# Kernel tuning notes

Hardware: AMD Instinct MI355X
Metric: run time of the kernel (lower is better)

Reference implementation:

```python
import jax, jax.numpy as jnp
import numpy as np

VOCAB = 32000
D = 512
H = 8
B = 1
SEQ = 4096
CHUNK = 1024  # max_len == chunk size


def _pe(seq, d):
    pos = np.arange(seq, dtype=np.float32)[:, None]
    div = np.exp(np.arange(0, d, 2, dtype=np.float32) * (-np.log(10000.0) / d))
    pe = np.zeros((seq, d), dtype=np.float32)
    pe[:, 0::2] = np.sin(pos * div)
    pe[:, 1::2] = np.cos(pos * div)
    return jnp.asarray(pe)


def _mha(x, w_in, b_in, w_out, b_out, h):
    # x: (..., L, d); attention along L, batched over leading dims.
    lead = x.shape[:-2]
    L, d = x.shape[-2], x.shape[-1]
    hd = d // h
    qkv = x @ w_in.T + b_in                      # (..., L, 3d)
    q, k, v = jnp.split(qkv, 3, axis=-1)
    q = q.reshape(lead + (L, h, hd))
    k = k.reshape(lead + (L, h, hd))
    v = v.reshape(lead + (L, h, hd))
    scores = jnp.einsum('...qhd,...khd->...hqk', q, k) * (1.0 / np.sqrt(hd))
    attn = jax.nn.softmax(scores, axis=-1)
    o = jnp.einsum('...hqk,...khd->...qhd', attn, v).reshape(lead + (L, d))
    return o @ w_out.T + b_out


def _ln(x, g, b, eps=1e-5):
    m = x.mean(-1, keepdims=True)
    v = x.var(-1, keepdims=True)
    return (x - m) / jnp.sqrt(v + eps) * g + b


def setup_inputs() -> dict:
    key = jax.random.key(0)
    ks = jax.random.split(key, 10)
    n = lambda k, s: jax.random.normal(k, s, jnp.float32) * 0.02
    return {
        'tokens': jax.random.randint(ks[0], (B, SEQ), 0, VOCAB),
        'emb': n(ks[1], (VOCAB, D)),
        'chunk_w_in': n(ks[2], (3 * D, D)), 'chunk_b_in': jnp.zeros((3 * D,), jnp.float32),
        'chunk_w_out': n(ks[3], (D, D)), 'chunk_b_out': jnp.zeros((D,), jnp.float32),
        'glob_w_in': n(ks[4], (3 * D, D)), 'glob_b_in': jnp.zeros((3 * D,), jnp.float32),
        'glob_w_out': n(ks[5], (D, D)), 'glob_b_out': jnp.zeros((D,), jnp.float32),
        'ln1_g': jnp.ones((D,), jnp.float32), 'ln1_b': jnp.zeros((D,), jnp.float32),
        'ffn_w1': n(ks[6], (4 * D, D)), 'ffn_b1': jnp.zeros((4 * D,), jnp.float32),
        'ffn_w2': n(ks[7], (D, 4 * D)), 'ffn_b2': jnp.zeros((D,), jnp.float32),
        'ln2_g': jnp.ones((D,), jnp.float32), 'ln2_b': jnp.zeros((D,), jnp.float32),
        'fc_w': n(ks[8], (VOCAB, D)), 'fc_b': jnp.zeros((VOCAB,), jnp.float32),
    }


def reference(tokens, emb, chunk_w_in, chunk_b_in, chunk_w_out, chunk_b_out,
              glob_w_in, glob_b_in, glob_w_out, glob_b_out,
              ln1_g, ln1_b, ffn_w1, ffn_b1, ffn_w2, ffn_b2,
              ln2_g, ln2_b, fc_w, fc_b):
    # embedding * sqrt(d) + sinusoidal positional encoding (dropout in eval = identity)
    x = emb[tokens] * np.sqrt(D).astype(np.float32) + _pe(SEQ, D)[None]  # (B, S, d)
    b, s, d = x.shape
    nc = s // CHUNK
    # BeamSplitter chunk stage: attend across the nc chunks at each intra-chunk position
    xc = x.reshape(b, nc, CHUNK, d).transpose(0, 2, 1, 3)   # (B, CHUNK, nc, d)
    ca = _mha(xc, chunk_w_in, chunk_b_in, chunk_w_out, chunk_b_out, H)
    ca = ca.transpose(0, 2, 1, 3).reshape(b, s, d)          # (B, S, d)
    # global stage: full attention over the sequence
    ga = _mha(ca, glob_w_in, glob_b_in, glob_w_out, glob_b_out, H)
    # post-norm transformer encoder layer
    x = _ln(x + ga, ln1_g, ln1_b)
    f = jax.nn.relu(x @ ffn_w1.T + ffn_b1) @ ffn_w2.T + ffn_b2
    x = _ln(x + f, ln2_g, ln2_b)
    return x @ fc_w.T + fc_b                                 # (B, S, VOCAB)
```

## Files before the change

kernel.cpp:

```cpp
#include <hip/hip_runtime.h>

typedef __attribute__((ext_vector_type(8))) short bf16x8;
typedef __attribute__((ext_vector_type(4))) float f32x4;
typedef unsigned short u16;

__device__ __forceinline__ u16 f2b(float f) {
  union { float f; unsigned u; } v; v.f = f;
  return (u16)((v.u + 0x7FFFu + ((v.u >> 16) & 1u)) >> 16);
}
__device__ __forceinline__ float b2f(u16 x) {
  union { unsigned u; float f; } v; v.u = (unsigned)x << 16; return v.f;
}

__device__ __forceinline__ void gload16(const void* g, void* l) {
  __builtin_amdgcn_global_load_lds((__attribute__((address_space(1))) void*)(g),
                                   (__attribute__((address_space(3))) void*)(l),
                                   16, 0, 0);
}

__device__ __forceinline__ void mbar() {
  asm volatile("" ::: "memory");
  __builtin_amdgcn_s_barrier();
  asm volatile("" ::: "memory");
}

__device__ __forceinline__ void cv1(const float4* __restrict__ s, u16* __restrict__ d, int i) {
  float4 v = s[i];
  unsigned long long pk = (unsigned long long)f2b(v.x) |
                          ((unsigned long long)f2b(v.y) << 16) |
                          ((unsigned long long)f2b(v.z) << 32) |
                          ((unsigned long long)f2b(v.w) << 48);
  *(unsigned long long*)(d + (size_t)i * 4) = pk;
}

__global__ __launch_bounds__(256)
void f2b_multi(const float4* s0, u16* d0, const float4* s1, u16* d1,
               const float4* s2, u16* d2, const float4* s3, u16* d3,
               const float4* s4, u16* d4, const float4* s5, u16* d5,
               const float4* s6, u16* d6) {
  int i = blockIdx.x * 256 + threadIdx.x;
  const int stride = gridDim.x * 256;
  for (; i < 5144576; i += stride) {
    int j = i;
    if (j < 196608) { cv1(s0, d0, j); continue; }
    j -= 196608;
    if (j < 65536) { cv1(s1, d1, j); continue; }
    j -= 65536;
    if (j < 196608) { cv1(s2, d2, j); continue; }
    j -= 196608;
    if (j < 65536) { cv1(s3, d3, j); continue; }
    j -= 65536;
    if (j < 262144) { cv1(s4, d4, j); continue; }
    j -= 262144;
    if (j < 262144) { cv1(s5, d5, j); continue; }
    j -= 262144;
    cv1(s6, d6, j);
  }
}

__global__ __launch_bounds__(256) void embed_pe(const int* __restrict__ tok,
    const float* __restrict__ emb, float* __restrict__ xf, u16* __restrict__ xb) {
  const int s = blockIdx.x;
  const int i = threadIdx.x;
  const int t = tok[s];
  const float div = __expf((float)(2 * i) * -0.017988946039015984f);
  const float ang = (float)s * div;
  const float sv = sinf(ang), cv = cosf(ang);
  const float* e = emb + (size_t)t * 512 + 2 * i;
  const float x0 = e[0] * 22.627416997969522f + sv;
  const float x1 = e[1] * 22.627416997969522f + cv;
  const size_t o = (size_t)s * 512 + 2 * i;
  xf[o] = x0; xf[o + 1] = x1;
  xb[o] = f2b(x0); xb[o + 1] = f2b(x1);
}

template<int BM, int RELU, int WF32, int WB16>
__global__ __launch_bounds__(256)
void gemm_bt(const u16* __restrict__ A, const u16* __restrict__ B,
             const float* __restrict__ bias, float* __restrict__ Cf,
             u16* __restrict__ Cb, int M, int N, int K)
{
  constexpr int MFR = BM / 32;
  __shared__ __align__(16) u16 As[BM * 64];
  __shared__ __align__(16) u16 Bs[128 * 64];
  const int tid = threadIdx.x;
  const int wid = tid >> 6, lane = tid & 63;
  const int lo = lane & 15, hi = lane >> 4;
  const int nbn = N >> 7;
  const int cpx = (int)gridDim.x >> 3;
  const int bid = blockIdx.x;
  const int swz = (bid & 7) * cpx + (bid >> 3);
  const int bi = swz / nbn, bj = swz - bi * nbn;
  const size_t row0 = (size_t)bi * BM, col0 = (size_t)bj << 7;
  const int wr = (wid >> 1) * (BM / 2), wc = (wid & 1) << 6;
  const int srow = (wid << 3) + (lane >> 3);
  const int scol = ((lane & 7) ^ (lane >> 3)) << 3;

  f32x4 acc[MFR][4] = {};

  auto rdA = [&](int row, int ks) -> bf16x8 {
    return *(const bf16x8*)((const char*)As + row * 128 + ((((ks << 2) | hi) ^ (row & 7)) << 4));
  };
  auto rdB = [&](int row, int ks) -> bf16x8 {
    return *(const bf16x8*)((const char*)Bs + row * 128 + ((((ks << 2) | hi) ^ (row & 7)) << 4));
  };

  for (int k0 = 0; k0 < K; k0 += 64) {
    __syncthreads();
#pragma unroll
    for (int p = 0; p < BM / 32; ++p)
      gload16(A + (row0 + srow + 32 * p) * (size_t)K + k0 + scol, &As[(wid * 8 + 32 * p) * 64]);
#pragma unroll
    for (int p = 0; p < 4; ++p)
      gload16(B + (col0 + srow + 32 * p) * (size_t)K + k0 + scol, &Bs[(wid * 8 + 32 * p) * 64]);
    __syncthreads();
#pragma unroll
    for (int ks = 0; ks < 2; ++ks) {
      bf16x8 af[MFR], bfr[4];
#pragma unroll
      for (int m = 0; m < MFR; ++m) af[m] = rdA(wr + m * 16 + lo, ks);
#pragma unroll
      for (int n = 0; n < 4; ++n) bfr[n] = rdB(wc + n * 16 + lo, ks);
#pragma unroll
      for (int m = 0; m < MFR; ++m)
#pragma unroll
        for (int n = 0; n < 4; ++n)
          acc[m][n] = __builtin_amdgcn_mfma_f32_16x16x32_bf16(af[m], bfr[n], acc[m][n], 0, 0, 0);
    }
  }

#pragma unroll
  for (int m = 0; m < MFR; ++m)
#pragma unroll
    for (int n = 0; n < 4; ++n) {
      const size_t c = col0 + wc + n * 16 + lo;
      const float bv = bias[c];
#pragma unroll
      for (int i = 0; i < 4; ++i) {
        const size_t r = row0 + wr + m * 16 + hi * 4 + i;
        float v = acc[m][n][i] + bv;
        if (RELU) v = fmaxf(v, 0.0f);
        if (WF32) Cf[r * (size_t)N + c] = v;
        if (WB16) Cb[r * (size_t)N + c] = f2b(v);
      }
    }
}

template<int KC>
__global__ __launch_bounds__(512, 2)
void gemm256(const u16* __restrict__ A, const u16* __restrict__ B,
             const float* __restrict__ bias, float* __restrict__ C,
             int M, int N)
{
  constexpr int T = KC / 64;
  __shared__ __align__(16) u16 LA[2][256 * 64];
  __shared__ __align__(16) u16 LB[2][256 * 64];
  const int tid = threadIdx.x;
  const int wid = tid >> 6, lane = tid & 63;
  const int lo = lane & 15, hi = lane >> 4;
  const int nbn = N >> 8;
  const int cpx = (int)gridDim.x >> 3;
  const int bid = blockIdx.x;
  const int swz = (bid & 7) * cpx + (bid >> 3);
  const int bi = swz / nbn, bj = swz - bi * nbn;
  const size_t row0 = (size_t)bi << 8, col0 = (size_t)bj << 8;
  const int wrow = (wid >> 2) << 7;
  const int wcol = (wid & 3) << 6;

  const int srow = (wid << 3) + (lane >> 3);
  const int scol = ((lane & 7) ^ (lane >> 3)) << 3;
  const u16* srcA = A + (row0 + srow) * (size_t)KC + scol;
  const u16* srcB = B + (col0 + srow) * (size_t)KC + scol;
  const int ldst = wid << 9;

  f32x4 acc[8][4] = {};

  auto stage = [&](int t, int b) {
    const size_t ko = (size_t)t * 64;
#pragma unroll
    for (int i = 0; i < 4; ++i)
      gload16(srcA + ko + (size_t)(i * 64) * KC, &LA[b][ldst + i * 4096]);
#pragma unroll
    for (int i = 0; i < 4; ++i)
      gload16(srcB + ko + (size_t)(i * 64) * KC, &LB[b][ldst + i * 4096]);
  };

  auto rd = [&](const u16* base, int row, int ks) -> bf16x8 {
    const int byte = row * 128 + ((((ks << 2) | hi) ^ (row & 7)) << 4);
    return *(const bf16x8*)((const char*)base + byte);
  };

  stage(0, 0);
  stage(1, 1);

  for (int t = 0; t < T; ++t) {
    const int b = t & 1;
    const u16* Ab = LA[b];
    const u16* Bb = LB[b];
    if (t + 1 < T) { asm volatile("s_waitcnt vmcnt(8)" ::: "memory"); }
    else           { asm volatile("s_waitcnt vmcnt(0)" ::: "memory"); }
    __builtin_amdgcn_sched_barrier(0);
    mbar();

    bf16x8 afr[4], bfr[4];
#pragma unroll
    for (int ks = 0; ks < 2; ++ks) {
#pragma unroll
      for (int m = 0; m < 4; ++m) afr[m] = rd(Ab, wrow + m * 16 + lo, ks);
#pragma unroll
      for (int n = 0; n < 4; ++n) bfr[n] = rd(Bb, wcol + n * 16 + lo, ks);
      mbar();
      asm volatile("s_waitcnt lgkmcnt(0)" ::: "memory");
      __builtin_amdgcn_sched_barrier(0);
      __builtin_amdgcn_s_setprio(1);
#pragma unroll
      for (int m = 0; m < 4; ++m)
#pragma unroll
        for (int n = 0; n < 4; ++n)
          acc[m][n] = __builtin_amdgcn_mfma_f32_16x16x32_bf16(afr[m], bfr[n], acc[m][n], 0, 0, 0);
      __builtin_amdgcn_s_setprio(0);
      mbar();
#pragma unroll
      for (int m = 0; m < 4; ++m) afr[m] = rd(Ab, wrow + (4 + m) * 16 + lo, ks);
      mbar();
      asm volatile("s_waitcnt lgkmcnt(0)" ::: "memory");
      __builtin_amdgcn_sched_barrier(0);
      __builtin_amdgcn_s_setprio(1);
#pragma unroll
      for (int m = 0; m < 4; ++m)
#pragma unroll
        for (int n = 0; n < 4; ++n)
          acc[4 + m][n] = __builtin_amdgcn_mfma_f32_16x16x32_bf16(afr[m], bfr[n], acc[4 + m][n], 0, 0, 0);
      __builtin_amdgcn_s_setprio(0);
      mbar();
    }
    if (t + 2 < T) stage(t + 2, b);
  }

#pragma unroll
  for (int m = 0; m < 8; ++m)
#pragma unroll
    for (int n = 0; n < 4; ++n) {
      const size_t c = col0 + wcol + n * 16 + lo;
      const float bv = bias[c];
#pragma unroll
      for (int i = 0; i < 4; ++i) {
        const size_t r = row0 + wrow + m * 16 + hi * 4 + i;
        C[r * (size_t)N + c] = acc[m][n][i] + bv;
      }
    }
}

__global__ __launch_bounds__(64)
void chunk_attn(const u16* __restrict__ qkv, u16* __restrict__ out) {
  const int p = blockIdx.x, h = blockIdx.y, d = threadIdx.x;
  float q[4], k[4], v[4];
#pragma unroll
  for (int c = 0; c < 4; ++c) {
    const u16* b = qkv + (size_t)((c << 10) + p) * 1536 + (h << 6) + d;
    q[c] = b2f(b[0]); k[c] = b2f(b[512]); v[c] = b2f(b[1024]);
  }
  float sc[4][4];
#pragma unroll
  for (int i = 0; i < 4; ++i)
#pragma unroll
    for (int j = 0; j < 4; ++j) sc[i][j] = q[i] * k[j];
#pragma unroll
  for (int mask = 1; mask < 64; mask <<= 1)
#pragma unroll
    for (int i = 0; i < 4; ++i)
#pragma unroll
      for (int j = 0; j < 4; ++j) sc[i][j] += __shfl_xor(sc[i][j], mask);
#pragma unroll
  for (int i = 0; i < 4; ++i) {
    float s0 = sc[i][0] * 0.125f, s1 = sc[i][1] * 0.125f,
          s2 = sc[i][2] * 0.125f, s3 = sc[i][3] * 0.125f;
    const float mx = fmaxf(fmaxf(s0, s1), fmaxf(s2, s3));
    const float e0 = __expf(s0 - mx), e1 = __expf(s1 - mx),
                e2 = __expf(s2 - mx), e3 = __expf(s3 - mx);
    const float inv = 1.0f / (e0 + e1 + e2 + e3);
    const float o = (e0 * v[0] + e1 * v[1] + e2 * v[2] + e3 * v[3]) * inv;
    out[(size_t)((i << 10) + p) * 512 + (h << 6) + d] = f2b(o);
  }
}

__global__ __launch_bounds__(512)
void flash_attn(const u16* __restrict__ qkv, u16* __restrict__ out) {
  __shared__ __align__(16) u16 Ks[64 * 64];
  __shared__ __align__(16) u16 Vt[64 * 64];
  __shared__ __align__(16) u16 Pp[8][16 * 64];
  const int tid = threadIdx.x, wid = tid >> 6, lane = tid & 63;
  const int lo = lane & 15, hi = lane >> 4;
  const int q0 = blockIdx.x << 7, h = blockIdx.y;
  const int hoff = h << 6;
  char* KsB = (char*)Ks; char* VtB = (char*)Vt;
  char* Pw = (char*)&Pp[wid][0];
  const int xsw = (lo & 7) << 4;
  constexpr float C1 = 0.18033688011112042f;

  bf16x8 qf[2];
#pragma unroll
  for (int kh = 0; kh < 2; ++kh)
    qf[kh] = *(const bf16x8*)(qkv + (size_t)(q0 + wid * 16 + lo) * 1536 + hoff + kh * 32 + hi * 8);

  f32x4 o[4] = {};
  float mr = -3e38f, lr = 0.f;

  const int krow = tid >> 3, kq = tid & 7;

  bf16x8 kpre = *(const bf16x8*)(qkv + (size_t)krow * 1536 + 512 + hoff + kq * 8);
  bf16x8 vpre = *(const bf16x8*)(qkv + (size_t)krow * 1536 + 1024 + hoff + kq * 8);

  for (int kv0 = 0; kv0 < 4096; kv0 += 64) {
    __syncthreads();
    *(bf16x8*)(KsB + ((krow * 128 + kq * 16) ^ ((krow & 7) << 4))) = kpre;
    {
      const unsigned* vp = (const unsigned*)&vpre;
      const int oddr = krow & 1;
      const unsigned t0 = oddr ? vp[0] : vp[2];
      const unsigned t1 = oddr ? vp[1] : vp[3];
      const unsigned r0 = (unsigned)__shfl_xor((int)t0, 8);
      const unsigned r1 = (unsigned)__shfl_xor((int)t1, 8);
      const unsigned E0 = oddr ? r0 : vp[0];
      const unsigned E1 = oddr ? r1 : vp[1];
      const unsigned O0 = oddr ? vp[2] : r0;
      const unsigned O1 = oddr ? vp[3] : r1;
      const int jp = krow & ~1;
      const int db = kq * 8 + oddr * 4;
      unsigned w0 = (E0 & 0xffffu) | (O0 << 16);
      unsigned w1 = (E0 >> 16) | (O0 & 0xffff0000u);
      unsigned w2 = (E1 & 0xffffu) | (O1 << 16);
      unsigned w3 = (E1 >> 16) | (O1 & 0xffff0000u);
      *(unsigned*)(VtB + (((db + 0) * 128 + 2 * jp) ^ (((db + 0) & 7) << 4))) = w0;
      *(unsigned*)(VtB + (((db + 1) * 128 + 2 * jp) ^ (((db + 1) & 7) << 4))) = w1;
      *(unsigned*)(VtB + (((db + 2) * 128 + 2 * jp) ^ (((db + 2) & 7) << 4))) = w2;
      *(unsigned*)(VtB + (((db + 3) * 128 + 2 * jp) ^ (((db + 3) & 7) << 4))) = w3;
    }
    __syncthreads();
    if (kv0 + 64 < 4096) {
      kpre = *(const bf16x8*)(qkv + (size_t)(kv0 + 64 + krow) * 1536 + 512 + hoff + kq * 8);
      vpre = *(const bf16x8*)(qkv + (size_t)(kv0 + 64 + krow) * 1536 + 1024 + hoff + kq * 8);
    }

    f32x4 s[4] = {};
#pragma unroll
    for (int n = 0; n < 4; ++n) {
      const int key = n * 16 + lo;
#pragma unroll
      for (int kh = 0; kh < 2; ++kh) {
        bf16x8 kf = *(const bf16x8*)(KsB + ((key * 128 + kh * 64 + hi * 16) ^ ((key & 7) << 4)));
        s[n] = __builtin_amdgcn_mfma_f32_16x16x32_bf16(kf, qf[kh], s[n], 0, 0, 0);
      }
    }

    float pm = s[0][0];
#pragma unroll
    for (int n = 0; n < 4; ++n)
#pragma unroll
      for (int i = 0; i < 4; ++i) pm = fmaxf(pm, s[n][i]);
    pm = fmaxf(pm, __shfl_xor(pm, 16));
    pm = fmaxf(pm, __shfl_xor(pm, 32));

    if (__any(pm > mr + 64.f)) {
      const float mn = fmaxf(mr, pm);
      const float sc = exp2f((mr - mn) * C1);
      mr = mn;
      lr *= sc;
#pragma unroll
      for (int i = 0; i < 4; ++i) {
        const float sq = __shfl(sc, hi * 4 + i);
#pragma unroll
        for (int n = 0; n < 4; ++n) o[n][i] *= sq;
      }
    }

    const float mc = mr * C1;
    float rs = 0.f;
    unsigned U[8];
#pragma unroll
    for (int n = 0; n < 4; ++n) {
      const float p0 = exp2f(fmaf(s[n][0], C1, -mc));
      const float p1 = exp2f(fmaf(s[n][1], C1, -mc));
      const float p2 = exp2f(fmaf(s[n][2], C1, -mc));
      const float p3 = exp2f(fmaf(s[n][3], C1, -mc));
      rs += (p0 + p1) + (p2 + p3);
      asm("v_cvt_pk_bf16_f32 %0, %1, %2" : "=v"(U[2 * n])     : "v"(p0), "v"(p1));
      asm("v_cvt_pk_bf16_f32 %0, %1, %2" : "=v"(U[2 * n + 1]) : "v"(p2), "v"(p3));
    }
    rs += __shfl_xor(rs, 16);
    rs += __shfl_xor(rs, 32);
    lr += rs;
#pragma unroll
    for (int n = 0; n < 4; ++n) {
      const int off = lo * 128 + ((n * 32 + hi * 8) ^ xsw);
      const unsigned long long dw = (unsigned long long)U[2 * n] |
                                    ((unsigned long long)U[2 * n + 1] << 32);
      *(unsigned long long*)(Pw + off) = dw;
    }

#pragma unroll
    for (int kh = 0; kh < 2; ++kh) {
      bf16x8 pa = *(const bf16x8*)(Pw + lo * 128 + ((kh * 64 + hi * 16) ^ xsw));
#pragma unroll
      for (int n = 0; n < 4; ++n) {
        const int vd = n * 16 + lo;
        bf16x8 vf = *(const bf16x8*)(VtB + ((vd * 128 + kh * 64 + hi * 16) ^ ((vd & 7) << 4)));
        o[n] = __builtin_amdgcn_mfma_f32_16x16x32_bf16(pa, vf, o[n], 0, 0, 0);
      }
    }
  }

#pragma unroll
  for (int i = 0; i < 4; ++i) {
    const float lq = __shfl(lr, hi * 4 + i);
    const float inv = 1.0f / lq;
    const int r = q0 + wid * 16 + hi * 4 + i;
#pragma unroll
    for (int n = 0; n < 4; ++n)
      out[(size_t)r * 512 + hoff + n * 16 + lo] = f2b(o[n][i] * inv);
  }
}

__global__ __launch_bounds__(256)
void add_ln(const float* __restrict__ a, const float* __restrict__ b,
            const float* __restrict__ g, const float* __restrict__ be,
            float* __restrict__ of, u16* __restrict__ ob) {
  const int wid = threadIdx.x >> 6, lane = threadIdx.x & 63;
  const int row = blockIdx.x * 4 + wid;
  const size_t base = (size_t)row * 512 + lane * 8;
  float4 a0 = *(const float4*)(a + base), a1 = *(const float4*)(a + base + 4);
  float4 b0 = *(const float4*)(b + base), b1 = *(const float4*)(b + base + 4);
  float x[8] = {a0.x + b0.x, a0.y + b0.y, a0.z + b0.z, a0.w + b0.w,
                a1.x + b1.x, a1.y + b1.y, a1.z + b1.z, a1.w + b1.w};
  float s = 0.f, sq = 0.f;
#pragma unroll
  for (int j = 0; j < 8; ++j) { s += x[j]; sq += x[j] * x[j]; }
#pragma unroll
  for (int mask = 1; mask < 64; mask <<= 1) {
    s += __shfl_xor(s, mask);
    sq += __shfl_xor(sq, mask);
  }
  const float mean = s * (1.0f / 512.0f);
  const float var = sq * (1.0f / 512.0f) - mean * mean;
  const float rstd = rsqrtf(var + 1e-5f);
  float4 g0 = *(const float4*)(g + lane * 8), g1 = *(const float4*)(g + lane * 8 + 4);
  float4 e0 = *(const float4*)(be + lane * 8), e1 = *(const float4*)(be + lane * 8 + 4);
  const float gg[8] = {g0.x, g0.y, g0.z, g0.w, g1.x, g1.y, g1.z, g1.w};
  const float bb[8] = {e0.x, e0.y, e0.z, e0.w, e1.x, e1.y, e1.z, e1.w};
#pragma unroll
  for (int j = 0; j < 8; ++j) {
    const float y = (x[j] - mean) * rstd * gg[j] + bb[j];
    of[base + j] = y;
    ob[base + j] = f2b(y);
  }
}

extern "C" void kernel_launch(void* const* d_in, const int* in_sizes, int n_in,
                              void* d_out, int out_size, void* d_ws, size_t ws_size,
                              hipStream_t stream) {
  (void)in_sizes; (void)n_in; (void)out_size; (void)ws_size;
  const int*   tokens = (const int*)d_in[0];
  const float* emb    = (const float*)d_in[1];
  const float* cwin   = (const float*)d_in[2];
  const float* cbin   = (const float*)d_in[3];
  const float* cwout  = (const float*)d_in[4];
  const float* cbout  = (const float*)d_in[5];
  const float* gwin   = (const float*)d_in[6];
  const float* gbin   = (const float*)d_in[7];
  const float* gwout  = (const float*)d_in[8];
  const float* gbout  = (const float*)d_in[9];
  const float* ln1g   = (const float*)d_in[10];
  const float* ln1b   = (const float*)d_in[11];
  const float* fw1    = (const float*)d_in[12];
  const float* fb1    = (const float*)d_in[13];
  const float* fw2    = (const float*)d_in[14];
  const float* fb2    = (const float*)d_in[15];
  const float* ln2g   = (const float*)d_in[16];
  const float* ln2b   = (const float*)d_in[17];
  const float* fcw    = (const float*)d_in[18];
  const float* fcb    = (const float*)d_in[19];
  float* out = (float*)d_out;

  char* ws = (char*)d_ws;
  size_t off = 0;
  auto alloc = [&](size_t bytes) -> void* {
    void* p = ws + off;
    off += (bytes + 255) & ~(size_t)255;
    return p;
  };
  u16*   xb    = (u16*)alloc((size_t)4096 * 512 * 2);
  float* xf    = (float*)alloc((size_t)4096 * 512 * 4);
  u16*   qkv1b = (u16*)alloc((size_t)4096 * 1536 * 2);
  u16*   at1   = (u16*)alloc((size_t)4096 * 512 * 2);
  u16*   cab   = (u16*)alloc((size_t)4096 * 512 * 2);
  u16*   qkv2  = (u16*)alloc((size_t)4096 * 1536 * 2);
  u16*   at2   = (u16*)alloc((size_t)4096 * 512 * 2);
  float* gaf   = (float*)alloc((size_t)4096 * 512 * 4);
  float* x1f   = (float*)alloc((size_t)4096 * 512 * 4);
  u16*   x1b   = (u16*)alloc((size_t)4096 * 512 * 2);
  u16*   f1b   = (u16*)alloc((size_t)4096 * 2048 * 2);
  float* ff    = (float*)alloc((size_t)4096 * 512 * 4);
  float* x2f   = (float*)alloc((size_t)4096 * 512 * 4);
  u16*   x2b   = (u16*)alloc((size_t)4096 * 512 * 2);
  u16*   wcinb  = (u16*)alloc((size_t)1536 * 512 * 2);
  u16*   wcoutb = (u16*)alloc((size_t)512 * 512 * 2);
  u16*   wginb  = (u16*)alloc((size_t)1536 * 512 * 2);
  u16*   wgoutb = (u16*)alloc((size_t)512 * 512 * 2);
  u16*   wf1b   = (u16*)alloc((size_t)2048 * 512 * 2);
  u16*   wf2b   = (u16*)alloc((size_t)512 * 2048 * 2);
  u16*   wfcb   = (u16*)alloc((size_t)32000 * 512 * 2);

  f2b_multi<<<2048, 256, 0, stream>>>(
      (const float4*)cwin, wcinb, (const float4*)cwout, wcoutb,
      (const float4*)gwin, wginb, (const float4*)gwout, wgoutb,
      (const float4*)fw1, wf1b, (const float4*)fw2, wf2b,
      (const float4*)fcw, wfcb);

  embed_pe<<<4096, 256, 0, stream>>>(tokens, emb, xf, xb);

  gemm_bt<128, 0, 0, 1><<<384, 256, 0, stream>>>(xb, wcinb, cbin, (float*)nullptr, qkv1b, 4096, 1536, 512);
  chunk_attn<<<dim3(1024, 8), 64, 0, stream>>>(qkv1b, at1);
  gemm_bt<64, 0, 0, 1><<<256, 256, 0, stream>>>(at1, wcoutb, cbout, (float*)nullptr, cab, 4096, 512, 512);

  gemm_bt<128, 0, 0, 1><<<384, 256, 0, stream>>>(cab, wginb, gbin, (float*)nullptr, qkv2, 4096, 1536, 512);
  flash_attn<<<dim3(32, 8), 512, 0, stream>>>(qkv2, at2);
  gemm_bt<64, 0, 1, 0><<<256, 256, 0, stream>>>(at2, wgoutb, gbout, gaf, (u16*)nullptr, 4096, 512, 512);

  add_ln<<<1024, 256, 0, stream>>>(xf, gaf, ln1g, ln1b, x1f, x1b);
  gemm_bt<128, 1, 0, 1><<<512, 256, 0, stream>>>(x1b, wf1b, fb1, (float*)nullptr, f1b, 4096, 2048, 512);
  gemm_bt<64, 0, 1, 0><<<256, 256, 0, stream>>>(f1b, wf2b, fb2, ff, (u16*)nullptr, 4096, 512, 2048);
  add_ln<<<1024, 256, 0, stream>>>(x1f, ff, ln2g, ln2b, x2f, x2b);

  gemm256<512><<<2000, 512, 0, stream>>>(x2b, wfcb, fcb, out, 4096, 32000);
}
```

Before: 474.1 us.

## Split-KV flash attention with merge, persistent vocab GEMM, fast sin/cos

Flash attention now runs over two halves of the key/value sequence as a third grid dimension, writing unnormalized fp32 partial outputs plus row max and sum. A new merge kernel combines the two halves into bf16, so twice as many blocks are available to fill the GPU. The vocab projection GEMM becomes a persistent kernel of 250 blocks. Each block keeps one 256-column B tile and loops over 8 row tiles, pipelining loads across tile boundaries and loading bias once. Embedding uses the fast __sinf/__cosf intrinsics, which are less accurate for large angles. The split adds fp32 partial traffic and an extra launch, and reuses the qkv1b and xb buffers as scratch.

```diff
diff --git a/kernel.cpp b/kernel.cpp
--- a/kernel.cpp
+++ b/kernel.cpp
@@ -65,7 +65,7 @@
   const int t = tok[s];
   const float div = __expf((float)(2 * i) * -0.017988946039015984f);
   const float ang = (float)s * div;
-  const float sv = sinf(ang), cv = cosf(ang);
+  const float sv = __sinf(ang), cv = __cosf(ang);
   const float* e = emb + (size_t)t * 512 + 2 * i;
   const float x0 = e[0] * 22.627416997969522f + sv;
   const float x1 = e[1] * 22.627416997969522f + cv;
@@ -148,41 +148,42 @@
 
 template<int KC>
 __global__ __launch_bounds__(512, 2)
-void gemm256(const u16* __restrict__ A, const u16* __restrict__ B,
-             const float* __restrict__ bias, float* __restrict__ C,
-             int M, int N)
+void gemm256p(const u16* __restrict__ A, const u16* __restrict__ B,
+              const float* __restrict__ bias, float* __restrict__ C, int N)
 {
-  constexpr int T = KC / 64;
   __shared__ __align__(16) u16 LA[2][256 * 64];
   __shared__ __align__(16) u16 LB[2][256 * 64];
   const int tid = threadIdx.x;
   const int wid = tid >> 6, lane = tid & 63;
   const int lo = lane & 15, hi = lane >> 4;
-  const int nbn = N >> 8;
-  const int cpx = (int)gridDim.x >> 3;
-  const int bid = blockIdx.x;
-  const int swz = (bid & 7) * cpx + (bid >> 3);
-  const int bi = swz / nbn, bj = swz - bi * nbn;
-  const size_t row0 = (size_t)bi << 8, col0 = (size_t)bj << 8;
+  const int b = blockIdx.x;
+  const int bj = b % 125, bi0 = b / 125;
+  const size_t col0 = (size_t)bj << 8;
   const int wrow = (wid >> 2) << 7;
   const int wcol = (wid & 3) << 6;
 
   const int srow = (wid << 3) + (lane >> 3);
   const int scol = ((lane & 7) ^ (lane >> 3)) << 3;
-  const u16* srcA = A + (row0 + srow) * (size_t)KC + scol;
   const u16* srcB = B + (col0 + srow) * (size_t)KC + scol;
   const int ldst = wid << 9;
 
+  float bv[4];
+#pragma unroll
+  for (int n = 0; n < 4; ++n) bv[n] = bias[col0 + wcol + n * 16 + lo];
+  asm volatile("" : "+v"(bv[0]), "+v"(bv[1]), "+v"(bv[2]), "+v"(bv[3]));
+
   f32x4 acc[8][4] = {};
 
-  auto stage = [&](int t, int b) {
-    const size_t ko = (size_t)t * 64;
+  auto stageAB = [&](int s) {
+    const int jj = s >> 3, tt = s & 7, buf = s & 1;
+    const u16* sA = A + ((size_t)((bi0 + 2 * jj) << 8) + srow) * KC + tt * 64 + scol;
 #pragma unroll
     for (int i = 0; i < 4; ++i)
-      gload16(srcA + ko + (size_t)(i * 64) * KC, &LA[b][ldst + i * 4096]);
+      gload16(sA + (size_t)(i * 64) * KC, &LA[buf][ldst + i * 4096]);
+    const u16* sB = srcB + tt * 64;
 #pragma unroll
     for (int i = 0; i < 4; ++i)
-      gload16(srcB + ko + (size_t)(i * 64) * KC, &LB[b][ldst + i * 4096]);
+      gload16(sB + (size_t)(i * 64) * KC, &LB[buf][ldst + i * 4096]);
   };
 
   auto rd = [&](const u16* base, int row, int ks) -> bf16x8 {
@@ -190,65 +191,73 @@
     return *(const bf16x8*)((const char*)base + byte);
   };
 
-  stage(0, 0);
-  stage(1, 1);
-
-  for (int t = 0; t < T; ++t) {
-    const int b = t & 1;
-    const u16* Ab = LA[b];
-    const u16* Bb = LB[b];
-    if (t + 1 < T) { asm volatile("s_waitcnt vmcnt(8)" ::: "memory"); }
-    else           { asm volatile("s_waitcnt vmcnt(0)" ::: "memory"); }
-    __builtin_amdgcn_sched_barrier(0);
-    mbar();
-
-    bf16x8 afr[4], bfr[4];
-#pragma unroll
-    for (int ks = 0; ks < 2; ++ks) {
-#pragma unroll
-      for (int m = 0; m < 4; ++m) afr[m] = rd(Ab, wrow + m * 16 + lo, ks);
-#pragma unroll
-      for (int n = 0; n < 4; ++n) bfr[n] = rd(Bb, wcol + n * 16 + lo, ks);
+  stageAB(0);
+  stageAB(1);
+
+  for (int j = 0; j < 8; ++j) {
+#pragma unroll
+    for (int t = 0; t < 8; ++t) {
+      const int s = j * 8 + t;
+      const u16* Ab = LA[s & 1];
+      const u16* Bb = LB[s & 1];
+      if (j > 0 && t <= 1)  { asm volatile("s_waitcnt vmcnt(40)" ::: "memory"); }
+      else if (s == 63)     { asm volatile("s_waitcnt vmcnt(0)" ::: "memory"); }
+      else                  { asm volatile("s_waitcnt vmcnt(8)" ::: "memory"); }
+      __builtin_amdgcn_sched_barrier(0);
       mbar();
-      asm volatile("s_waitcnt lgkmcnt(0)" ::: "memory");
-      __builtin_amdgcn_sched_barrier(0);
-      __builtin_amdgcn_s_setprio(1);
-#pragma unroll
-      for (int m = 0; m < 4; ++m)
-#pragma unroll
-        for (int n = 0; n < 4; ++n)
-          acc[m][n] = __builtin_amdgcn_mfma_f32_16x16x32_bf16(afr[m], bfr[n], acc[m][n], 0, 0, 0);
-      __builtin_amdgcn_s_setprio(0);
-      mbar();
-#pragma unroll
-      for (int m = 0; m < 4; ++m) afr[m] = rd(Ab, wrow + (4 + m) * 16 + lo, ks);
-      mbar();
-      asm volatile("s_waitcnt lgkmcnt(0)" ::: "memory");
-      __builtin_amdgcn_sched_barrier(0);
-      __builtin_amdgcn_s_setprio(1);
-#pragma unroll
-      for (int m = 0; m < 4; ++m)
-#pragma unroll
-        for (int n = 0; n < 4; ++n)
-          acc[4 + m][n] = __builtin_amdgcn_mfma_f32_16x16x32_bf16(afr[m], bfr[n], acc[4 + m][n], 0, 0, 0);
-      __builtin_amdgcn_s_setprio(0);
-      mbar();
-    }
-    if (t + 2 < T) stage(t + 2, b);
-  }
-
-#pragma unroll
-  for (int m = 0; m < 8; ++m)
-#pragma unroll
-    for (int n = 0; n < 4; ++n) {
-      const size_t c = col0 + wcol + n * 16 + lo;
-      const float bv = bias[c];
-#pragma unroll
-      for (int i = 0; i < 4; ++i) {
-        const size_t r = row0 + wrow + m * 16 + hi * 4 + i;
-        C[r * (size_t)N + c] = acc[m][n][i] + bv;
+
+      bf16x8 afr[4], bfr[4];
+#pragma unroll
+      for (int ks = 0; ks < 2; ++ks) {
+#pragma unroll
+        for (int m = 0; m < 4; ++m) afr[m] = rd(Ab, wrow + m * 16 + lo, ks);
+#pragma unroll
+        for (int n = 0; n < 4; ++n) bfr[n] = rd(Bb, wcol + n * 16 + lo, ks);
+        mbar();
+        asm volatile("s_waitcnt lgkmcnt(0)" ::: "memory");
+        __builtin_amdgcn_sched_barrier(0);
+        __builtin_amdgcn_s_setprio(1);
+#pragma unroll
+        for (int m = 0; m < 4; ++m)
+#pragma unroll
+          for (int n = 0; n < 4; ++n)
+            acc[m][n] = __builtin_amdgcn_mfma_f32_16x16x32_bf16(afr[m], bfr[n], acc[m][n], 0, 0, 0);
+        __builtin_amdgcn_s_setprio(0);
+        mbar();
+#pragma unroll
+        for (int m = 0; m < 4; ++m) afr[m] = rd(Ab, wrow + (4 + m) * 16 + lo, ks);
+        mbar();
+        asm volatile("s_waitcnt lgkmcnt(0)" ::: "memory");
+        __builtin_amdgcn_sched_barrier(0);
+        __builtin_amdgcn_s_setprio(1);
+#pragma unroll
+        for (int m = 0; m < 4; ++m)
+#pragma unroll
+          for (int n = 0; n < 4; ++n)
+            acc[4 + m][n] = __builtin_amdgcn_mfma_f32_16x16x32_bf16(afr[m], bfr[n], acc[4 + m][n], 0, 0, 0);
+        __builtin_amdgcn_s_setprio(0);
+        mbar();
       }
-    }
+      if (s + 2 < 64) stageAB(s + 2);
+    }
+    const size_t row0 = (size_t)((bi0 + 2 * j) << 8);
+#pragma unroll
+    for (int m = 0; m < 8; ++m)
+#pragma unroll
+      for (int n = 0; n < 4; ++n) {
+        const size_t c = col0 + wcol + n * 16 + lo;
+#pragma unroll
+        for (int i = 0; i < 4; ++i) {
+          const size_t r = row0 + wrow + m * 16 + hi * 4 + i;
+          C[r * (size_t)N + c] = acc[m][n][i] + bv[n];
+        }
+      }
+#pragma unroll
+    for (int m = 0; m < 8; ++m)
+#pragma unroll
+      for (int n = 0; n < 4; ++n)
+        acc[m][n] = f32x4{0.f, 0.f, 0.f, 0.f};
+  }
 }
 
 __global__ __launch_bounds__(64)
@@ -284,14 +293,16 @@
   }
 }
 
-__global__ __launch_bounds__(512)
-void flash_attn(const u16* __restrict__ qkv, u16* __restrict__ out) {
+__global__ __launch_bounds__(512, 4)
+void flash_attn(const u16* __restrict__ qkv, float* __restrict__ pO,
+                float* __restrict__ pm, float* __restrict__ pl) {
   __shared__ __align__(16) u16 Ks[64 * 64];
   __shared__ __align__(16) u16 Vt[64 * 64];
   __shared__ __align__(16) u16 Pp[8][16 * 64];
   const int tid = threadIdx.x, wid = tid >> 6, lane = tid & 63;
   const int lo = lane & 15, hi = lane >> 4;
-  const int q0 = blockIdx.x << 7, h = blockIdx.y;
+  const int q0 = blockIdx.x << 7, h = blockIdx.y, z = blockIdx.z;
+  const int kvb = z << 11;
   const int hoff = h << 6;
   char* KsB = (char*)Ks; char* VtB = (char*)Vt;
   char* Pw = (char*)&Pp[wid][0];
@@ -308,10 +319,10 @@
 
   const int krow = tid >> 3, kq = tid & 7;
 
-  bf16x8 kpre = *(const bf16x8*)(qkv + (size_t)krow * 1536 + 512 + hoff + kq * 8);
-  bf16x8 vpre = *(const bf16x8*)(qkv + (size_t)krow * 1536 + 1024 + hoff + kq * 8);
-
-  for (int kv0 = 0; kv0 < 4096; kv0 += 64) {
+  bf16x8 kpre = *(const bf16x8*)(qkv + (size_t)(kvb + krow) * 1536 + 512 + hoff + kq * 8);
+  bf16x8 vpre = *(const bf16x8*)(qkv + (size_t)(kvb + krow) * 1536 + 1024 + hoff + kq * 8);
+
+  for (int kv0 = kvb; kv0 < kvb + 2048; kv0 += 64) {
     __syncthreads();
     *(bf16x8*)(KsB + ((krow * 128 + kq * 16) ^ ((krow & 7) << 4))) = kpre;
     {
@@ -337,7 +348,7 @@
       *(unsigned*)(VtB + (((db + 3) * 128 + 2 * jp) ^ (((db + 3) & 7) << 4))) = w3;
     }
     __syncthreads();
-    if (kv0 + 64 < 4096) {
+    if (kv0 + 64 < kvb + 2048) {
       kpre = *(const bf16x8*)(qkv + (size_t)(kv0 + 64 + krow) * 1536 + 512 + hoff + kq * 8);
       vpre = *(const bf16x8*)(qkv + (size_t)(kv0 + 64 + krow) * 1536 + 1024 + hoff + kq * 8);
     }
@@ -353,16 +364,16 @@
       }
     }
 
-    float pm = s[0][0];
+    float pmx = s[0][0];
 #pragma unroll
     for (int n = 0; n < 4; ++n)
 #pragma unroll
-      for (int i = 0; i < 4; ++i) pm = fmaxf(pm, s[n][i]);
-    pm = fmaxf(pm, __shfl_xor(pm, 16));
-    pm = fmaxf(pm, __shfl_xor(pm, 32));
-
-    if (__any(pm > mr + 64.f)) {
-      const float mn = fmaxf(mr, pm);
+      for (int i = 0; i < 4; ++i) pmx = fmaxf(pmx, s[n][i]);
+    pmx = fmaxf(pmx, __shfl_xor(pmx, 16));
+    pmx = fmaxf(pmx, __shfl_xor(pmx, 32));
+
+    if (__any(pmx > mr + 64.f)) {
+      const float mn = fmaxf(mr, pmx);
       const float sc = exp2f((mr - mn) * C1);
       mr = mn;
       lr *= sc;
@@ -412,13 +423,39 @@
 
 #pragma unroll
   for (int i = 0; i < 4; ++i) {
-    const float lq = __shfl(lr, hi * 4 + i);
-    const float inv = 1.0f / lq;
     const int r = q0 + wid * 16 + hi * 4 + i;
 #pragma unroll
     for (int n = 0; n < 4; ++n)
-      out[(size_t)r * 512 + hoff + n * 16 + lo] = f2b(o[n][i] * inv);
-  }
+      pO[((size_t)z * 4096 + r) * 512 + hoff + n * 16 + lo] = o[n][i];
+  }
+  if (hi == 0) {
+    const int r = q0 + wid * 16 + lo;
+    pm[(z * 8 + h) * 4096 + r] = mr;
+    pl[(z * 8 + h) * 4096 + r] = lr;
+  }
+}
+
+__global__ __launch_bounds__(256)
+void attn_merge(const float* __restrict__ pO, const float* __restrict__ pm,
+                const float* __restrict__ pl, u16* __restrict__ out) {
+  constexpr float C1 = 0.18033688011112042f;
+  const int tid = threadIdx.x, lane = tid & 63, w = tid >> 6;
+  const int row = blockIdx.x * 4 + w;
+  const int d = lane * 8, h = lane >> 3;
+  const float m0 = pm[h * 4096 + row], m1 = pm[(8 + h) * 4096 + row];
+  const float l0 = pl[h * 4096 + row], l1 = pl[(8 + h) * 4096 + row];
+  const float M = fmaxf(m0, m1);
+  const float w0 = exp2f((m0 - M) * C1), w1 = exp2f((m1 - M) * C1);
+  const float inv = 1.0f / (l0 * w0 + l1 * w1);
+  const float* a = pO + (size_t)row * 512 + d;
+  const float* b = pO + ((size_t)4096 + row) * 512 + d;
+  float4 a0 = *(const float4*)a, a1 = *(const float4*)(a + 4);
+  float4 b0 = *(const float4*)b, b1 = *(const float4*)(b + 4);
+  const float A[8] = {a0.x, a0.y, a0.z, a0.w, a1.x, a1.y, a1.z, a1.w};
+  const float Bv[8] = {b0.x, b0.y, b0.z, b0.w, b1.x, b1.y, b1.z, b1.w};
+#pragma unroll
+  for (int j = 0; j < 8; ++j)
+    out[(size_t)row * 512 + d + j] = f2b((A[j] * w0 + Bv[j] * w1) * inv);
 }
 
 __global__ __launch_bounds__(256)
@@ -510,6 +547,10 @@
   u16*   wf2b   = (u16*)alloc((size_t)512 * 2048 * 2);
   u16*   wfcb   = (u16*)alloc((size_t)32000 * 512 * 2);
 
+  float* pO = (float*)qkv1b;
+  float* pm = (float*)xb;
+  float* pl = pm + 2 * 8 * 4096;
+
   f2b_multi<<<2048, 256, 0, stream>>>(
       (const float4*)cwin, wcinb, (const float4*)cwout, wcoutb,
       (const float4*)gwin, wginb, (const float4*)gwout, wgoutb,
@@ -523,7 +564,8 @@
   gemm_bt<64, 0, 0, 1><<<256, 256, 0, stream>>>(at1, wcoutb, cbout, (float*)nullptr, cab, 4096, 512, 512);
 
   gemm_bt<128, 0, 0, 1><<<384, 256, 0, stream>>>(cab, wginb, gbin, (float*)nullptr, qkv2, 4096, 1536, 512);
-  flash_attn<<<dim3(32, 8), 512, 0, stream>>>(qkv2, at2);
+  flash_attn<<<dim3(32, 8, 2), 512, 0, stream>>>(qkv2, pO, pm, pl);
+  attn_merge<<<1024, 256, 0, stream>>>(pO, pm, pl, at2);
   gemm_bt<64, 0, 1, 0><<<256, 256, 0, stream>>>(at2, wgoutb, gbout, gaf, (u16*)nullptr, 4096, 512, 512);
 
   add_ln<<<1024, 256, 0, stream>>>(xf, gaf, ln1g, ln1b, x1f, x1b);
@@ -531,5 +573,5 @@
   gemm_bt<64, 0, 1, 0><<<256, 256, 0, stream>>>(f1b, wf2b, fb2, ff, (u16*)nullptr, 4096, 512, 2048);
   add_ln<<<1024, 256, 0, stream>>>(x1f, ff, ln2g, ln2b, x2f, x2b);
 
-  gemm256<512><<<2000, 512, 0, stream>>>(x2b, wfcb, fcb, out, 4096, 32000);
-}
+  gemm256p<512><<<250, 512, 0, stream>>>(x2b, wfcb, fcb, out, 32000);
+}
```

Result: slower. 494.2 us (+4.3%).
